# Optimization experiments

Hardware: AMD Instinct MI355X
Metric: run time of the kernel (lower is better)

The kernel has to match this reference:

```python
import jax, jax.numpy as jnp
import numpy as np

U, B, D = 1024, 8, 512
H, HD = 8, 64
CL, RC = 64, 4            # chunk length, right-context per chunk
C = U // CL               # 16 chunks
R, S, M = C * RC, C, C - 1
Q, KV = R + U + S, M + R + U
PE = 2 * U - 1
NEG_INF = -1e8


def _chunk_mask():
    # True = disallowed connection. Query rows = [right_context(R), utterance(U), summary(S)];
    # key cols = [memory(M), right_context(R), utterance(U)].
    mask = np.ones((Q, KV), dtype=bool)
    for c in range(C):
        cols = []
        cols += list(range(0, c))                                  # memory of preceding chunks
        cols += list(range(M + c * RC, M + (c + 1) * RC))          # own right context
        u0 = max(0, c - 1) * CL                                    # one left-context chunk
        cols += list(range(M + R + u0, M + R + (c + 1) * CL))      # utterance up to own chunk
        cols = np.array(cols)
        rows = np.concatenate([
            np.arange(c * RC, (c + 1) * RC),                       # right-context queries
            np.arange(R + c * CL, R + (c + 1) * CL),               # utterance queries
            np.array([R + U + c]),                                 # summary query
        ])
        mask[np.ix_(rows, cols)] = False
    return jnp.asarray(mask)


def _xavier(key, shape):
    fan_in, fan_out = shape[-1], shape[0]
    a = (6.0 / (fan_in + fan_out)) ** 0.5
    return jax.random.uniform(key, shape, jnp.float32, -a, a)


def setup_inputs() -> dict:
    key = jax.random.key(0)
    ks = jax.random.split(key, 16)
    return {
        "utterance": jax.random.normal(ks[0], (U, B, D), jnp.float32),
        "lengths": jax.random.randint(ks[1], (B,), U // 2, U + 1),
        "right_context": jax.random.normal(ks[2], (R, B, D), jnp.float32),
        "summary": jax.random.normal(ks[3], (S, B, D), jnp.float32),
        "memory": jax.random.normal(ks[4], (M, B, D), jnp.float32),
        "attention_mask": _chunk_mask(),
        "pos_emb": jax.random.normal(ks[5], (PE, D), jnp.float32),
        "W_kv": _xavier(ks[6], (2 * D, D)),
        "b_kv": jnp.zeros((2 * D,), jnp.float32),
        "W_q": _xavier(ks[7], (D, D)),
        "b_q": jnp.zeros((D,), jnp.float32),
        "W_out": _xavier(ks[8], (D, D)),
        "b_out": jnp.zeros((D,), jnp.float32),
        "W_pos": _xavier(ks[9], (D, D)),
        "pos_bias_u": _xavier(ks[10], (H, HD)),
        "pos_bias_v": _xavier(ks[11], (H, HD)),
    }


def reference(utterance, lengths, right_context, summary, memory, attention_mask,
              pos_emb, W_kv, b_kv, W_q, b_q, W_out, b_out, W_pos,
              pos_bias_u, pos_bias_v):
    u_len, b, d = utterance.shape
    r, m, s = right_context.shape[0], memory.shape[0], summary.shape[0]
    h = pos_bias_u.shape[0]
    hd = d // h
    scaling = hd ** -0.5

    query = jnp.concatenate([right_context, utterance, summary], 0) @ W_q.T + b_q   # (Q,B,D)
    kv = jnp.concatenate([memory, right_context, utterance], 0) @ W_kv.T + b_kv     # (KV,B,2D)
    key_t, val_t = kv[..., :d], kv[..., d:]
    q_len, kv_len = query.shape[0], key_t.shape[0]

    k = key_t.reshape(kv_len, b, h, hd).transpose(1, 2, 0, 3)   # (B,H,KV,hd)
    v = val_t.reshape(kv_len, b, h, hd).transpose(1, 2, 0, 3)   # (B,H,KV,hd)
    q = query.reshape(q_len, b, h, hd)                           # (Q,B,H,hd)

    qu = (q + pos_bias_u).transpose(1, 2, 0, 3)                  # (B,H,Q,hd)
    matrix_ac = jnp.einsum('bhqe,bhke->bhqk', qu, k)             # (B,H,Q,KV)

    qv = (q[r:r + u_len] + pos_bias_v).transpose(1, 2, 0, 3)     # (B,H,U,hd)
    pe_len = pos_emb.shape[0]
    pos = (pos_emb @ W_pos.T).reshape(pe_len, h, hd).transpose(1, 0, 2)  # (H,PE,hd)
    bd_u = jnp.einsum('bhue,hpe->bhup', qv, pos)                 # (B,H,U,PE)

    # rel_shift: out[u, j] = in[u, U-1-u+j]
    out_len = pe_len - (u_len - 1)
    idx = (u_len - 1) - jnp.arange(u_len)[:, None] + jnp.arange(out_len)[None, :]
    bd_u = jnp.take_along_axis(bd_u, idx[None, None], axis=-1)   # (B,H,U,out_len)

    matrix_bd = jnp.zeros_like(matrix_ac).at[:, :, r:r + u_len, m + r:].set(bd_u)
    w = (matrix_ac + matrix_bd) * scaling

    w = jnp.where(attention_mask[None, None], NEG_INF, w)
    pad = jnp.arange(kv_len)[None, :] >= (kv_len - u_len + lengths)[:, None]  # (B,KV)
    w = jnp.where(pad[:, None, None, :], NEG_INF, w)

    probs = jax.nn.softmax(w, axis=-1)
    attn = jnp.einsum('bhqk,bhke->bhqe', probs, v)               # (B,H,Q,hd)
    attn = attn.transpose(2, 0, 1, 3).reshape(q_len, b, d)       # (Q,B,D)

    out_ru = attn[:r + u_len] @ W_out.T + b_out                  # (R+U,B,D)
    out_mem = jnp.clip(attn[r + u_len:], -10.0, 10.0)            # (S,B,D); tanh_on_mem=False
    return out_ru, out_mem
```

## Files before the change

### kernel.cpp

```cpp
#include <hip/hip_runtime.h>
#include <hip/hip_bf16.h>

typedef __hip_bfloat16 bf16;
typedef __attribute__((ext_vector_type(8))) short short8v;
typedef __attribute__((ext_vector_type(4))) float float4v;

#define UU 1024
#define BB 8
#define DD 512
#define HH 8
#define HD 64
#define RR 64
#define SS 16
#define MM 15
#define QQ 1104
#define KVL 1103
#define PEL 2047
#define NU 1536
#define MU 8952

#define AS1 __attribute__((address_space(1)))
#define AS3 __attribute__((address_space(3)))

__device__ __forceinline__ float lo16(unsigned u) { return __uint_as_float(u << 16); }
__device__ __forceinline__ float hi16(unsigned u) { return __uint_as_float(u & 0xffff0000u); }
__device__ __forceinline__ unsigned pk2(float a, float b) {
  unsigned short x = __builtin_bit_cast(unsigned short, __float2bfloat16(a));
  unsigned short y = __builtin_bit_cast(unsigned short, __float2bfloat16(b));
  return (unsigned)x | ((unsigned)y << 16);
}

__device__ __forceinline__ void nt_st_bf16(bf16* p, float v) {
  bf16 t = __float2bfloat16(v);
  __builtin_nontemporal_store(__builtin_bit_cast(short, t), (short*)p);
}
__device__ __forceinline__ void nt_st_f32(float* p, float v) {
  __builtin_nontemporal_store(v, p);
}

struct PackDesc {
  const void* src[16];
  unsigned int srcoff[16];
  unsigned int dstoff[16];
  unsigned int cum[17];
};

__global__ __launch_bounds__(256) void pack_all(PackDesc d, bf16* base,
                                                const void* __restrict__ probe,
                                                int* __restrict__ flagout,
                                                int nchunks) {
  __shared__ int wsum[4];
  const unsigned short* p = (const unsigned short*)probe;
  int big = 0;
  for (int i = threadIdx.x; i < 4096; i += 256)
    big += (((p[i] >> 7) & 0xFF) >= 137) ? 1 : 0;
  #pragma unroll
  for (int off = 32; off; off >>= 1) big += __shfl_down(big, off);
  if ((threadIdx.x & 63) == 0) wsum[threadIdx.x >> 6] = big;
  __syncthreads();
  const int flag = (wsum[0] + wsum[1] + wsum[2] + wsum[3] < 16) ? 1 : 0;
  if (threadIdx.x == 0 && blockIdx.x == 0) *flagout = flag;

  int g = blockIdx.x * 256 + threadIdx.x;
  if (g >= nchunks) return;
  int s = 0;
  #pragma unroll
  for (int i = 1; i < 17; ++i) s += (g >= d.cum[i]) ? 1 : 0;
  unsigned local = (g - d.cum[s]) * 8u;
  bf16* dst = base + d.dstoff[s] + local;
  if (flag) {
    const uint4 v = *(const uint4*)((const bf16*)d.src[s] + d.srcoff[s] + local);
    *(uint4*)dst = v;
  } else {
    const float* fp = (const float*)d.src[s] + d.srcoff[s] + local;
    uint4 o;
    o.x = pk2(fp[0], fp[1]);
    o.y = pk2(fp[2], fp[3]);
    o.z = pk2(fp[4], fp[5]);
    o.w = pk2(fp[6], fp[7]);
    *(uint4*)dst = o;
  }
}

struct GemmP {
  const bf16* X; const bf16* W; const bf16* bias; void* out;
  int M, N, K; const int* outf;
};

__global__ __launch_bounds__(256, 3) void gemm_dual(GemmP g0, GemmP g1, int ysplit) {
  __shared__ bf16 As[64 * 128];
  __shared__ bf16 Bs[128 * 128];
  GemmP g; int bm, bn;
  if ((int)blockIdx.y < ysplit) {
    g = g0;
    int bi = (int)blockIdx.y * (int)gridDim.x + (int)blockIdx.x;
    int nbn = g0.N >> 7;
    int j = bi >> 3;
    int bmi = (bi & 7) + (j / nbn) * 8;
    int bni = j % nbn;
    if (bmi >= ((g0.M + 63) >> 6)) return;
    bm = bmi * 64; bn = bni * 128;
  } else {
    g = g1;
    int nt = g1.N >> 7;
    int bi = ((int)blockIdx.y - ysplit) * gridDim.x + blockIdx.x;
    if (bi >= ((g1.M + 63) >> 6) * nt) return;
    bm = (bi / nt) * 64; bn = (bi % nt) * 128;
  }
  const int tid = threadIdx.x;
  const int lane = tid & 63, wv = tid >> 6;
  const int wr = wv >> 1, wc = wv & 1;
  const int l4 = lane >> 4;
  const int lb = lane & 15;
  const int quad = lane >> 4, l15 = lane & 15;

  float4v acc[2][4] = {};

  for (int kb = 0; kb < g.K; kb += 128) {
    #pragma unroll
    for (int i = 0; i < 4; ++i) {
      int r = wv * 16 + i * 4 + l4;
      int gm = bm + r; if (gm > g.M - 1) gm = g.M - 1;
      const bf16* src = g.X + (size_t)gm * g.K + kb + ((lb ^ (r & 15)) * 8);
      __builtin_amdgcn_global_load_lds((const AS1 void*)src,
                                       (AS3 void*)&As[(wv * 16 + i * 4) * 128], 16, 0, 0);
    }
    #pragma unroll
    for (int i = 0; i < 8; ++i) {
      int r = wv * 32 + i * 4 + l4;
      int gn = bn + r; if (gn > g.N - 1) gn = g.N - 1;
      const bf16* src = g.W + (size_t)gn * g.K + kb + ((lb ^ (r & 15)) * 8);
      __builtin_amdgcn_global_load_lds((const AS1 void*)src,
                                       (AS3 void*)&Bs[(wv * 32 + i * 4) * 128], 16, 0, 0);
    }
    __syncthreads();
    #pragma unroll
    for (int ki = 0; ki < 4; ++ki) {
      const int slot = ((ki * 4 + quad) ^ l15) * 8;
      short8v a[2], bq[4];
      #pragma unroll
      for (int t = 0; t < 2; ++t)
        a[t] = *(const short8v*)&As[(wr * 32 + t * 16 + l15) * 128 + slot];
      #pragma unroll
      for (int t = 0; t < 4; ++t)
        bq[t] = *(const short8v*)&Bs[(wc * 64 + t * 16 + l15) * 128 + slot];
      #pragma unroll
      for (int mt = 0; mt < 2; ++mt)
        #pragma unroll
        for (int nt = 0; nt < 4; ++nt)
          acc[mt][nt] = __builtin_amdgcn_mfma_f32_16x16x32_bf16(
              a[mt], bq[nt], acc[mt][nt], 0, 0, 0);
    }
    __syncthreads();
  }

  const bool as_bf16 = (g.outf == nullptr) ? true : (*g.outf != 0);
  #pragma unroll
  for (int mt = 0; mt < 2; ++mt) {
    #pragma unroll
    for (int r = 0; r < 4; ++r) {
      int gm = bm + wr * 32 + mt * 16 + quad * 4 + r;
      if (gm >= g.M) continue;
      #pragma unroll
      for (int nt = 0; nt < 4; ++nt) {
        int gn = bn + wc * 64 + nt * 16 + l15;
        float v = acc[mt][nt][r];
        if (g.bias) v += __bfloat162float(g.bias[gn]);
        size_t o = (size_t)gm * g.N + gn;
        if (as_bf16) nt_st_bf16((bf16*)g.out + o, v);
        else         nt_st_f32((float*)g.out + o, v);
      }
    }
  }
}

__global__ __launch_bounds__(512, 2) void gemm8(
    const bf16* __restrict__ XUp, const bf16* __restrict__ Wcatp,
    const bf16* __restrict__ bcatp, bf16* __restrict__ qkvp,
    const bf16* __restrict__ posecp, const bf16* __restrict__ Wpospp,
    bf16* __restrict__ posp) {
  __shared__ bf16 smem[65536];
  const int tid = threadIdx.x;
  const int lane = tid & 63, wv = tid >> 6;
  const int wr = wv >> 2, wc = wv & 3;
  const int quad = lane >> 4, l15 = lane & 15;

  const bf16 *gX, *gW, *gB; bf16* gO; int gM, gN, bm, bn;
  const int bid = (int)blockIdx.x;
  if (bid < 210) {
    int xcd = bid & 7, j = bid >> 3;
    int wg = (xcd < 2 ? xcd * 27 : 54 + (xcd - 2) * 26) + j;
    bm = (wg / 6) * 256; bn = (wg % 6) * 256;
    gX = XUp; gW = Wcatp; gB = bcatp; gO = qkvp; gM = MU; gN = NU;
  } else {
    gX = posecp; gW = Wpospp; gB = nullptr; gO = posp; gM = 191; gN = 512;
    bm = 0; bn = (bid - 210) * 256;
  }

  bf16* A0 = smem;
  bf16* B0 = smem + 32768;

  auto stage = [&](const bf16* src, int rbase, int Mlim, bf16* dst, int kb) {
    #pragma unroll
    for (int j = 0; j < 2; ++j) {
      int rl = j * 128 + wv * 16 + (lane >> 2);
      int gr = rbase + rl; if (gr > Mlim - 1) gr = Mlim - 1;
      int kc = ((lane & 3) ^ ((rl >> 1) & 3)) * 8;
      const bf16* s = src + (size_t)gr * 512 + kb + kc;
      __builtin_amdgcn_global_load_lds((const AS1 void*)s,
                                       (AS3 void*)(dst + (j * 128 + wv * 16) * 32), 16, 0, 0);
    }
  };

  float4v acc[8][4] = {};
  const int pos8 = (quad ^ ((l15 >> 1) & 3)) * 8;

  stage(gX, bm, gM, A0, 0);          stage(gW, bn, gN, B0, 0);
  stage(gX, bm, gM, A0 + 8192, 32);  stage(gW, bn, gN, B0 + 8192, 32);
  stage(gX, bm, gM, A0 + 16384, 64); stage(gW, bn, gN, B0 + 16384, 64);
  asm volatile("s_waitcnt vmcnt(8)" ::: "memory");
  asm volatile("s_barrier" ::: "memory");

  #pragma unroll
  for (int s = 0; s < 16; ++s) {
    if (s + 3 < 16) {
      stage(gX, bm, gM, A0 + ((s + 3) & 3) * 8192, (s + 3) * 32);
      stage(gW, bn, gN, B0 + ((s + 3) & 3) * 8192, (s + 3) * 32);
    }
    const bf16* As = A0 + (s & 3) * 8192;
    const bf16* Bs = B0 + (s & 3) * 8192;
    short8v al[8], bl[4];
    #pragma unroll
    for (int i = 0; i < 8; ++i)
      al[i] = *(const short8v*)&As[(wr * 128 + i * 16 + l15) * 32 + pos8];
    #pragma unroll
    for (int j = 0; j < 4; ++j)
      bl[j] = *(const short8v*)&Bs[(wc * 64 + j * 16 + l15) * 32 + pos8];
    asm volatile("s_barrier" ::: "memory");
    __builtin_amdgcn_s_setprio(1);
    #pragma unroll
    for (int i = 0; i < 8; ++i)
      #pragma unroll
      for (int j = 0; j < 4; ++j)
        acc[i][j] = __builtin_amdgcn_mfma_f32_16x16x32_bf16(al[i], bl[j], acc[i][j], 0, 0, 0);
    __builtin_amdgcn_s_setprio(0);
    if (s <= 12)      asm volatile("s_waitcnt vmcnt(8)" ::: "memory");
    else if (s == 13) asm volatile("s_waitcnt vmcnt(4)" ::: "memory");
    else if (s == 14) asm volatile("s_waitcnt vmcnt(0)" ::: "memory");
    if (s < 15)       asm volatile("s_barrier" ::: "memory");
  }

  #pragma unroll
  for (int mf = 0; mf < 8; ++mf) {
    #pragma unroll
    for (int r = 0; r < 4; ++r) {
      int gm = bm + wr * 128 + mf * 16 + quad * 4 + r;
      if (gm >= gM) continue;
      #pragma unroll
      for (int nf = 0; nf < 4; ++nf) {
        int gn = bn + wc * 64 + nf * 16 + l15;
        float v = acc[mf][nf][r];
        if (gB) v += __bfloat162float(gB[gn]);
        gO[(size_t)gm * gN + gn] = __float2bfloat16(v);
      }
    }
  }
}

__device__ __forceinline__ int gcol(int row, int c, int u0, int ncols) {
  if (row < c) return row;
  if (row < c + 4) return 15 + 4 * c + (row - c);
  if (row < ncols) return 79 + u0 + (row - c - 4);
  return 0;
}

__global__ __launch_bounds__(256, 2) void attn_chunk(
    const bf16* __restrict__ qkv, const bf16* __restrict__ pos,
    const bf16* __restrict__ pbu, const bf16* __restrict__ pbv,
    const int* __restrict__ lengths, bf16* __restrict__ attn,
    const int* __restrict__ flag, void* __restrict__ dout) {
  __shared__ char lds[65536];
  bf16* Vs   = (bf16*)(lds);
  bf16* Aqu  = (bf16*)(lds + 19456);
  bf16* Kt   = (bf16*)(lds + 29696);
  bf16* Aqv  = (bf16*)(lds + 32768);
  bf16* Psl  = (bf16*)(lds + 40960);
  bf16* Eb   = (bf16*)(lds + 49152);
  bf16* Pp   = (bf16*)(lds + 19456);
  float* wred  = (float*)(lds + 46336);
  float* rstat = (float*)(lds + 47616);

  const int idx = blockIdx.x;
  const int h = idx & 7, b = (idx >> 3) & 7, c = idx >> 6;
  const int u0 = c ? (c - 1) * 64 : 0;
  const int nut = c ? 128 : 64;
  const int ncols = c + 4 + nut;
  const int q0 = c ? 63 : 127;
  const int tid = threadIdx.x, lane = tid & 63, wv = tid >> 6;
  const int quad = lane >> 4, l15 = lane & 15, key = l15 & 7;
  const int lenlim = lengths[b] - u0;
  const bool obf = (*flag != 0);

  {
    int lr = lane >> 3;
    int sbr = (lane & 7) ^ lr;
    for (int i = wv; i < 19; i += 4) {
      int row = i * 8 + lr;
      int g = gcol(row, c, u0, ncols);
      int sbv = (lane & 7) ^ (i & 7);
      const bf16* src = qkv + ((size_t)(g * 8 + b)) * NU + 1024 + h * 64 + sbv * 8;
      __builtin_amdgcn_global_load_lds((const AS1 void*)src, (AS3 void*)(Vs + i * 512), 16, 0, 0);
    }
    for (int i = wv; i < 24; i += 4) {
      int p = i * 8 + lr;
      const bf16* src = pos + (size_t)p * 512 + h * 64 + sbr * 8;
      __builtin_amdgcn_global_load_lds((const AS1 void*)src, (AS3 void*)(Psl + i * 512), 16, 0, 0);
    }
  }
  for (int id = tid; id < 1152; id += 256) {
    bool isv = id >= 640;
    int lid = isv ? id - 640 : id;
    int m = lid >> 3, ec = lid & 7;
    int qrow;
    if (isv) qrow = 64 + 64 * c + m;
    else qrow = (m < 64) ? (64 + 64 * c + m)
              : (m < 68) ? (4 * c + (m - 64))
              : (m == 68) ? (1088 + c) : 0;
    const uint4 qa = *(const uint4*)(qkv + ((size_t)((qrow + 15) * 8 + b)) * NU + h * 64 + ec * 8);
    const uint4 ba = *(const uint4*)((isv ? pbv : pbu) + h * 64 + ec * 8);
    uint4 o;
    o.x = pk2(lo16(qa.x) + lo16(ba.x), hi16(qa.x) + hi16(ba.x));
    o.y = pk2(lo16(qa.y) + lo16(ba.y), hi16(qa.y) + hi16(ba.y));
    o.z = pk2(lo16(qa.z) + lo16(ba.z), hi16(qa.z) + hi16(ba.z));
    o.w = pk2(lo16(qa.w) + lo16(ba.w), hi16(qa.w) + hi16(ba.w));
    *(uint4*)((isv ? Aqv : Aqu) + m * 64 + (ec ^ (m & 7)) * 8) = o;
  }
  __syncthreads();

  float4v eacc[4][3];
  #pragma unroll
  for (int mt = 0; mt < 4; ++mt)
    #pragma unroll
    for (int i = 0; i < 3; ++i) eacc[mt][i] = (float4v){0.f, 0.f, 0.f, 0.f};
  {
    short8v av[4][2];
    #pragma unroll
    for (int mt = 0; mt < 4; ++mt)
      #pragma unroll
      for (int ks = 0; ks < 2; ++ks)
        av[mt][ks] = *(const short8v*)&Aqv[(mt * 16 + l15) * 64 + ((ks * 4 + quad) ^ key) * 8];
    #pragma unroll
    for (int nti = 0; nti < 3; ++nti) {
      int nt = wv + nti * 4;
      short8v b0 = *(const short8v*)&Psl[(nt * 16 + l15) * 64 + (quad ^ key) * 8];
      short8v b1 = *(const short8v*)&Psl[(nt * 16 + l15) * 64 + ((4 + quad) ^ key) * 8];
      #pragma unroll
      for (int mt = 0; mt < 4; ++mt) {
        eacc[mt][nti] = __builtin_amdgcn_mfma_f32_16x16x32_bf16(av[mt][0], b0, eacc[mt][nti], 0, 0, 0);
        eacc[mt][nti] = __builtin_amdgcn_mfma_f32_16x16x32_bf16(av[mt][1], b1, eacc[mt][nti], 0, 0, 0);
      }
    }
  }
  __syncthreads();

  {
    int lr = lane >> 3, sbr = (lane & 7) ^ lr;
    for (int i = wv; i < 19; i += 4) {
      int row = i * 8 + lr;
      int g = gcol(row, c, u0, ncols);
      const bf16* src = qkv + ((size_t)(g * 8 + b)) * NU + 512 + h * 64 + sbr * 8;
      __builtin_amdgcn_global_load_lds((const AS1 void*)src, (AS3 void*)(Kt + i * 512), 16, 0, 0);
    }
  }
  #pragma unroll
  for (int nti = 0; nti < 3; ++nti) {
    int p = (wv + nti * 4) * 16 + l15;
    #pragma unroll
    for (int mt = 0; mt < 4; ++mt)
      #pragma unroll
      for (int r = 0; r < 4; ++r) {
        int m = mt * 16 + quad * 4 + r;
        int jl = p - q0 + m;
        if (jl >= 0 && jl < nut)
          Eb[m * 128 + (jl ^ (((m >> 2) & 7) << 4))] = __float2bfloat16(eacc[mt][nti][r]);
      }
  }
  __syncthreads();

  const int nnt = (wv < 2) ? 3 : 2;
  float4v sacc[5][3];
  #pragma unroll
  for (int mt = 0; mt < 5; ++mt)
    #pragma unroll
    for (int i = 0; i < 3; ++i) sacc[mt][i] = (float4v){0.f, 0.f, 0.f, 0.f};
  {
    short8v au[5][2];
    #pragma unroll
    for (int mt = 0; mt < 5; ++mt)
      #pragma unroll
      for (int ks = 0; ks < 2; ++ks)
        au[mt][ks] = *(const short8v*)&Aqu[(mt * 16 + l15) * 64 + ((ks * 4 + quad) ^ key) * 8];
    #pragma unroll
    for (int nti = 0; nti < 3; ++nti) {
      if (nti < nnt) {
        int nt = wv + nti * 4;
        short8v b0 = *(const short8v*)&Kt[(nt * 16 + l15) * 64 + (quad ^ key) * 8];
        short8v b1 = *(const short8v*)&Kt[(nt * 16 + l15) * 64 + ((4 + quad) ^ key) * 8];
        #pragma unroll
        for (int mt = 0; mt < 5; ++mt) {
          sacc[mt][nti] = __builtin_amdgcn_mfma_f32_16x16x32_bf16(au[mt][0], b0, sacc[mt][nti], 0, 0, 0);
          sacc[mt][nti] = __builtin_amdgcn_mfma_f32_16x16x32_bf16(au[mt][1], b1, sacc[mt][nti], 0, 0, 0);
        }
      }
    }
  }
  __syncthreads();

  #pragma unroll
  for (int nti = 0; nti < 3; ++nti) {
    if (nti < nnt) {
      int colv = (wv + nti * 4) * 16 + l15;
      int jl = colv - (c + 4);
      bool cvalid = (colv < ncols) && !(jl >= 0 && jl >= lenlim);
      #pragma unroll
      for (int mt = 0; mt < 5; ++mt)
        #pragma unroll
        for (int r = 0; r < 4; ++r) {
          float s = sacc[mt][nti][r];
          if (cvalid) {
            if (mt < 4 && jl >= 0) {
              int m = mt * 16 + quad * 4 + r;
              s += __bfloat162float(Eb[m * 128 + (jl ^ (((m >> 2) & 7) << 4))]);
            }
            s *= 0.125f;
          } else s = -1e30f;
          sacc[mt][nti][r] = s;
        }
    }
  }

  {
    #pragma unroll
    for (int mt = 0; mt < 5; ++mt)
      #pragma unroll
      for (int r = 0; r < 4; ++r) {
        float v = -3e38f;
        #pragma unroll
        for (int nti = 0; nti < 3; ++nti)
          if (nti < nnt) v = fmaxf(v, sacc[mt][nti][r]);
        v = fmaxf(v, __shfl_xor(v, 1));
        v = fmaxf(v, __shfl_xor(v, 2));
        v = fmaxf(v, __shfl_xor(v, 4));
        v = fmaxf(v, __shfl_xor(v, 8));
        if (l15 == 0) wred[(mt * 16 + quad * 4 + r) * 4 + wv] = v;
      }
  }
  __syncthreads();
  if (tid < 80)
    rstat[tid] = fmaxf(fmaxf(wred[tid * 4], wred[tid * 4 + 1]),
                       fmaxf(wred[tid * 4 + 2], wred[tid * 4 + 3]));
  __syncthreads();

  {
    float rmx[5][4], rsum[5][4];
    #pragma unroll
    for (int mt = 0; mt < 5; ++mt)
      #pragma unroll
      for (int r = 0; r < 4; ++r) {
        rmx[mt][r] = rstat[mt * 16 + quad * 4 + r];
        rsum[mt][r] = 0.f;
      }
    #pragma unroll
    for (int nti = 0; nti < 3; ++nti) {
      if (nti < nnt) {
        int colv = (wv + nti * 4) * 16 + l15;
        #pragma unroll
        for (int mt = 0; mt < 5; ++mt)
          #pragma unroll
          for (int r = 0; r < 4; ++r) {
            float p = __expf(sacc[mt][nti][r] - rmx[mt][r]);
            Pp[(mt * 16 + quad * 4 + r) * 168 + colv] = __float2bfloat16(p);
            rsum[mt][r] += p;
          }
      }
    }
    #pragma unroll
    for (int mt = 0; mt < 5; ++mt)
      #pragma unroll
      for (int r = 0; r < 4; ++r) {
        float v = rsum[mt][r];
        v += __shfl_xor(v, 1);
        v += __shfl_xor(v, 2);
        v += __shfl_xor(v, 4);
        v += __shfl_xor(v, 8);
        if (l15 == 0) wred[(mt * 16 + quad * 4 + r) * 4 + wv] = v;
      }
  }
  __syncthreads();
  if (tid < 80)
    rstat[tid] = 1.f / (wred[tid * 4] + wred[tid * 4 + 1] + wred[tid * 4 + 2] + wred[tid * 4 + 3]);
  __syncthreads();

  const int kmax = (ncols + 31) >> 5;
  float4v oacc[5];
  #pragma unroll
  for (int mt = 0; mt < 5; ++mt) oacc[mt] = (float4v){0.f, 0.f, 0.f, 0.f};
  const int ehi = (wv * 16 + l15) >> 3, elo = l15 & 7;
  for (int ks = 0; ks < kmax; ++ks) {
    short8v bq;
    const int blk = ehi ^ ((ks * 4 + quad) & 7);
    #pragma unroll
    for (int j = 0; j < 8; ++j)
      bq[j] = ((const short*)Vs)[(ks * 32 + quad * 8 + j) * 64 + blk * 8 + elo];
    #pragma unroll
    for (int mt = 0; mt < 5; ++mt) {
      short8v af = *(const short8v*)&Pp[(mt * 16 + l15) * 168 + ks * 32 + quad * 8];
      oacc[mt] = __builtin_amdgcn_mfma_f32_16x16x32_bf16(af, bq, oacc[mt], 0, 0, 0);
    }
  }

  #pragma unroll
  for (int mt = 0; mt < 5; ++mt) {
    #pragma unroll
    for (int r = 0; r < 4; ++r) {
      int m = mt * 16 + quad * 4 + r;
      if (m >= 69) continue;
      float o = oacc[mt][r] * rstat[m];
      if (m < 68) {
        int qrow = (m < 64) ? (64 + 64 * c + m) : (4 * c + (m - 64));
        attn[((size_t)(qrow * 8 + b)) * 512 + h * 64 + wv * 16 + l15] = __float2bfloat16(o);
      } else {
        float v = fminf(fmaxf(o, -10.f), 10.f);
        size_t oi = (size_t)1088 * 8 * 512 + ((size_t)(c * 8 + b)) * 512 + h * 64 + wv * 16 + l15;
        if (obf) nt_st_bf16((bf16*)dout + oi, v);
        else     nt_st_f32((float*)dout + oi, v);
      }
    }
  }
}

static inline int cdiv(int a, int b) { return (a + b - 1) / b; }

extern "C" void kernel_launch(void* const* d_in, const int* in_sizes, int n_in,
                              void* d_out, int out_size, void* d_ws, size_t ws_size,
                              hipStream_t stream) {
  const void* utter = d_in[0];
  const int*  lens  = (const int*)d_in[1];
  const void* rctx  = d_in[2];
  const void* summ  = d_in[3];
  const void* memry = d_in[4];
  const void* pose  = d_in[6];
  const void* W_kv  = d_in[7];
  const void* b_kv  = d_in[8];
  const void* W_q   = d_in[9];
  const void* b_q   = d_in[10];
  const void* W_out = d_in[11];
  const void* b_out = d_in[12];
  const void* W_pos = d_in[13];
  const void* pbu   = d_in[14];
  const void* pbv   = d_in[15];

  const unsigned SZ_MM = MM * BB * DD;
  const unsigned SZ_RC = RR * BB * DD;
  const unsigned SZ_UT = UU * BB * DD;
  const unsigned SZ_SM = SS * BB * DD;
  const unsigned N_XU  = SZ_MM + SZ_RC + SZ_UT + SZ_SM;
  const unsigned SZ_PS = 191 * DD;

  int*  flag = (int*)d_ws;
  bf16* base = (bf16*)((char*)d_ws + 64);
  unsigned off = 0;
  bf16* XU    = base + off; unsigned o_XU    = off; off += N_XU;
  bf16* posec = base + off; unsigned o_posec = off; off += 192 * DD;
  bf16* Wcat  = base + off; unsigned o_Wcat  = off; off += (unsigned)NU * DD;
  bf16* bcat  = base + off; unsigned o_bcat  = off; off += NU;
  bf16* Woutp = base + off; unsigned o_Wout  = off; off += DD * DD;
  bf16* boutp = base + off; unsigned o_bout  = off; off += DD;
  bf16* Wposp = base + off; unsigned o_Wpos  = off; off += DD * DD;
  bf16* pbuc  = base + off; unsigned o_pbu   = off; off += DD;
  bf16* pbvc  = base + off; unsigned o_pbv   = off; off += DD;
  bf16* qkv   = base + off; off += (unsigned)(MU + 8) * NU;
  bf16* pos   = base + off; off += 192 * DD;
  bf16* attn  = base + off; off += QQ * BB * DD;

  PackDesc pd;
  const void* srcs[14]  = {memry, rctx, utter, summ, pose,
                           W_q, W_kv, b_q, b_kv, W_out, b_out, W_pos, pbu, pbv};
  unsigned    soffs[14] = {0, 0, 0, 0, 896u * DD, 0, 0, 0, 0, 0, 0, 0, 0, 0};
  unsigned    doffs[14] = {o_XU, o_XU + SZ_MM, o_XU + SZ_MM + SZ_RC,
                           o_XU + SZ_MM + SZ_RC + SZ_UT, o_posec,
                           o_Wcat, o_Wcat + DD * DD, o_bcat, o_bcat + DD,
                           o_Wout, o_bout, o_Wpos, o_pbu, o_pbv};
  unsigned    ns[14]    = {SZ_MM, SZ_RC, SZ_UT, SZ_SM, SZ_PS,
                           DD * DD, 2 * DD * DD, DD, 2 * DD,
                           DD * DD, DD, DD * DD, DD, DD};
  unsigned cum = 0;
  for (int i = 0; i < 14; ++i) {
    pd.src[i] = srcs[i]; pd.srcoff[i] = soffs[i]; pd.dstoff[i] = doffs[i];
    pd.cum[i] = cum; cum += ns[i] / 8;
  }
  pd.src[14] = pbv; pd.srcoff[14] = 0; pd.dstoff[14] = o_pbv;
  pd.src[15] = pbv; pd.srcoff[15] = 0; pd.dstoff[15] = o_pbv;
  pd.cum[14] = cum; pd.cum[15] = cum; pd.cum[16] = cum;
  int nchunks = (int)cum;
  pack_all<<<dim3(cdiv(nchunks, 256)), dim3(256), 0, stream>>>(pd, base, utter, flag, nchunks);

  gemm8<<<dim3(212), dim3(512), 0, stream>>>(XU, Wcat, bcat, qkv, posec, Wposp, pos);

  attn_chunk<<<dim3(1024), dim3(256), 0, stream>>>(qkv, pos, pbuc, pbvc, lens, attn,
                                                   flag, d_out);

  GemmP go{attn, Woutp, boutp, d_out, (RR + UU) * BB, DD, DD, flag};
  gemm_dual<<<dim3(4, 136), dim3(256), 0, stream>>>(go, go, 136);
}
```

Baseline: 196.7 us.

## Partition attention score tiles by query rows per wave to avoid cross-wave softmax reductions

Work in the chunk attention kernel is now split across waves by query-row tile instead of key-column tile. Each wave computes a full row of scores, with the key-column loop bounded by the actual column count, so softmax max and sum reductions stay within the wave. This removes the LDS scratch round-trip and several __syncthreads barriers. The cost is load imbalance: with five row tiles over four waves, wave 0 does two tiles while the others do one, and it raises per-wave accumulator register use.

```diff
diff --git a/kernel.cpp b/kernel.cpp
--- a/kernel.cpp
+++ b/kernel.cpp
@@ -287,7 +287,6 @@
   bf16* Psl  = (bf16*)(lds + 40960);
   bf16* Eb   = (bf16*)(lds + 49152);
   bf16* Pp   = (bf16*)(lds + 19456);
-  float* wred  = (float*)(lds + 46336);
   float* rstat = (float*)(lds + 47616);
 
   const int idx = blockIdx.x;
@@ -300,6 +299,7 @@
   const int quad = lane >> 4, l15 = lane & 15, key = l15 & 7;
   const int lenlim = lengths[b] - u0;
   const bool obf = (*flag != 0);
+  const int ktp = ((ncols + 31) >> 5) * 2;
 
   {
     int lr = lane >> 3;
@@ -337,28 +337,20 @@
   }
   __syncthreads();
 
-  float4v eacc[4][3];
-  #pragma unroll
-  for (int mt = 0; mt < 4; ++mt)
-    #pragma unroll
-    for (int i = 0; i < 3; ++i) eacc[mt][i] = (float4v){0.f, 0.f, 0.f, 0.f};
+  float4v eacc[12];
+  #pragma unroll
+  for (int i = 0; i < 12; ++i) eacc[i] = (float4v){0.f, 0.f, 0.f, 0.f};
   {
-    short8v av[4][2];
-    #pragma unroll
-    for (int mt = 0; mt < 4; ++mt)
-      #pragma unroll
-      for (int ks = 0; ks < 2; ++ks)
-        av[mt][ks] = *(const short8v*)&Aqv[(mt * 16 + l15) * 64 + ((ks * 4 + quad) ^ key) * 8];
-    #pragma unroll
-    for (int nti = 0; nti < 3; ++nti) {
-      int nt = wv + nti * 4;
-      short8v b0 = *(const short8v*)&Psl[(nt * 16 + l15) * 64 + (quad ^ key) * 8];
-      short8v b1 = *(const short8v*)&Psl[(nt * 16 + l15) * 64 + ((4 + quad) ^ key) * 8];
-      #pragma unroll
-      for (int mt = 0; mt < 4; ++mt) {
-        eacc[mt][nti] = __builtin_amdgcn_mfma_f32_16x16x32_bf16(av[mt][0], b0, eacc[mt][nti], 0, 0, 0);
-        eacc[mt][nti] = __builtin_amdgcn_mfma_f32_16x16x32_bf16(av[mt][1], b1, eacc[mt][nti], 0, 0, 0);
-      }
+    short8v av[2];
+    #pragma unroll
+    for (int ks = 0; ks < 2; ++ks)
+      av[ks] = *(const short8v*)&Aqv[(wv * 16 + l15) * 64 + ((ks * 4 + quad) ^ key) * 8];
+    #pragma unroll
+    for (int nti = 0; nti < 12; ++nti) {
+      short8v b0 = *(const short8v*)&Psl[(nti * 16 + l15) * 64 + (quad ^ key) * 8];
+      short8v b1 = *(const short8v*)&Psl[(nti * 16 + l15) * 64 + ((4 + quad) ^ key) * 8];
+      eacc[nti] = __builtin_amdgcn_mfma_f32_16x16x32_bf16(av[0], b0, eacc[nti], 0, 0, 0);
+      eacc[nti] = __builtin_amdgcn_mfma_f32_16x16x32_bf16(av[1], b1, eacc[nti], 0, 0, 0);
     }
   }
   __syncthreads();
@@ -373,132 +365,133 @@
     }
   }
   #pragma unroll
-  for (int nti = 0; nti < 3; ++nti) {
-    int p = (wv + nti * 4) * 16 + l15;
-    #pragma unroll
-    for (int mt = 0; mt < 4; ++mt)
-      #pragma unroll
-      for (int r = 0; r < 4; ++r) {
-        int m = mt * 16 + quad * 4 + r;
-        int jl = p - q0 + m;
-        if (jl >= 0 && jl < nut)
-          Eb[m * 128 + (jl ^ (((m >> 2) & 7) << 4))] = __float2bfloat16(eacc[mt][nti][r]);
-      }
+  for (int nti = 0; nti < 12; ++nti) {
+    int p = nti * 16 + l15;
+    #pragma unroll
+    for (int r = 0; r < 4; ++r) {
+      int m = wv * 16 + quad * 4 + r;
+      int jl = p - q0 + m;
+      if (jl >= 0 && jl < nut)
+        Eb[m * 128 + (jl ^ (((m >> 2) & 7) << 4))] = __float2bfloat16(eacc[nti][r]);
+    }
   }
   __syncthreads();
 
-  const int nnt = (wv < 2) ? 3 : 2;
-  float4v sacc[5][3];
-  #pragma unroll
-  for (int mt = 0; mt < 5; ++mt)
-    #pragma unroll
-    for (int i = 0; i < 3; ++i) sacc[mt][i] = (float4v){0.f, 0.f, 0.f, 0.f};
+  float4v sacc[2][10];
+  #pragma unroll
+  for (int ti = 0; ti < 2; ++ti)
+    #pragma unroll
+    for (int i = 0; i < 10; ++i) sacc[ti][i] = (float4v){0.f, 0.f, 0.f, 0.f};
   {
-    short8v au[5][2];
-    #pragma unroll
-    for (int mt = 0; mt < 5; ++mt)
-      #pragma unroll
-      for (int ks = 0; ks < 2; ++ks)
-        au[mt][ks] = *(const short8v*)&Aqu[(mt * 16 + l15) * 64 + ((ks * 4 + quad) ^ key) * 8];
-    #pragma unroll
-    for (int nti = 0; nti < 3; ++nti) {
-      if (nti < nnt) {
-        int nt = wv + nti * 4;
-        short8v b0 = *(const short8v*)&Kt[(nt * 16 + l15) * 64 + (quad ^ key) * 8];
-        short8v b1 = *(const short8v*)&Kt[(nt * 16 + l15) * 64 + ((4 + quad) ^ key) * 8];
+    short8v au[2][2];
+    #pragma unroll
+    for (int ti = 0; ti < 2; ++ti) {
+      int tt = wv + ti * 4;
+      if (tt < 5) {
         #pragma unroll
-        for (int mt = 0; mt < 5; ++mt) {
-          sacc[mt][nti] = __builtin_amdgcn_mfma_f32_16x16x32_bf16(au[mt][0], b0, sacc[mt][nti], 0, 0, 0);
-          sacc[mt][nti] = __builtin_amdgcn_mfma_f32_16x16x32_bf16(au[mt][1], b1, sacc[mt][nti], 0, 0, 0);
+        for (int ks = 0; ks < 2; ++ks)
+          au[ti][ks] = *(const short8v*)&Aqu[(tt * 16 + l15) * 64 + ((ks * 4 + quad) ^ key) * 8];
+      }
+    }
+    #pragma unroll
+    for (int nti = 0; nti < 10; ++nti) {
+      if (nti < ktp) {
+        short8v b0 = *(const short8v*)&Kt[(nti * 16 + l15) * 64 + (quad ^ key) * 8];
+        short8v b1 = *(const short8v*)&Kt[(nti * 16 + l15) * 64 + ((4 + quad) ^ key) * 8];
+        #pragma unroll
+        for (int ti = 0; ti < 2; ++ti) {
+          int tt = wv + ti * 4;
+          if (tt < 5) {
+            sacc[ti][nti] = __builtin_amdgcn_mfma_f32_16x16x32_bf16(au[ti][0], b0, sacc[ti][nti], 0, 0, 0);
+            sacc[ti][nti] = __builtin_amdgcn_mfma_f32_16x16x32_bf16(au[ti][1], b1, sacc[ti][nti], 0, 0, 0);
+          }
         }
       }
     }
   }
-  __syncthreads();
-
-  #pragma unroll
-  for (int nti = 0; nti < 3; ++nti) {
-    if (nti < nnt) {
-      int colv = (wv + nti * 4) * 16 + l15;
+
+  #pragma unroll
+  for (int nti = 0; nti < 10; ++nti) {
+    if (nti < ktp) {
+      int colv = nti * 16 + l15;
       int jl = colv - (c + 4);
       bool cvalid = (colv < ncols) && !(jl >= 0 && jl >= lenlim);
       #pragma unroll
-      for (int mt = 0; mt < 5; ++mt)
-        #pragma unroll
-        for (int r = 0; r < 4; ++r) {
-          float s = sacc[mt][nti][r];
-          if (cvalid) {
-            if (mt < 4 && jl >= 0) {
-              int m = mt * 16 + quad * 4 + r;
-              s += __bfloat162float(Eb[m * 128 + (jl ^ (((m >> 2) & 7) << 4))]);
-            }
-            s *= 0.125f;
-          } else s = -1e30f;
-          sacc[mt][nti][r] = s;
+      for (int ti = 0; ti < 2; ++ti) {
+        int tt = wv + ti * 4;
+        if (tt < 5) {
+          #pragma unroll
+          for (int r = 0; r < 4; ++r) {
+            float s = sacc[ti][nti][r];
+            if (cvalid) {
+              if (tt < 4 && jl >= 0) {
+                int m = tt * 16 + quad * 4 + r;
+                s += __bfloat162float(Eb[m * 128 + (jl ^ (((m >> 2) & 7) << 4))]);
+              }
+              s *= 0.125f;
+            } else s = -1e30f;
+            sacc[ti][nti][r] = s;
+          }
         }
-    }
-  }
-
-  {
-    #pragma unroll
-    for (int mt = 0; mt < 5; ++mt)
+      }
+    }
+  }
+
+  float rmx[2][4], rsum[2][4];
+  #pragma unroll
+  for (int ti = 0; ti < 2; ++ti) {
+    int tt = wv + ti * 4;
+    if (tt < 5) {
       #pragma unroll
       for (int r = 0; r < 4; ++r) {
         float v = -3e38f;
         #pragma unroll
-        for (int nti = 0; nti < 3; ++nti)
-          if (nti < nnt) v = fmaxf(v, sacc[mt][nti][r]);
+        for (int nti = 0; nti < 10; ++nti)
+          if (nti < ktp) v = fmaxf(v, sacc[ti][nti][r]);
         v = fmaxf(v, __shfl_xor(v, 1));
         v = fmaxf(v, __shfl_xor(v, 2));
         v = fmaxf(v, __shfl_xor(v, 4));
         v = fmaxf(v, __shfl_xor(v, 8));
-        if (l15 == 0) wred[(mt * 16 + quad * 4 + r) * 4 + wv] = v;
-      }
+        rmx[ti][r] = v;
+        rsum[ti][r] = 0.f;
+      }
+    }
   }
   __syncthreads();
-  if (tid < 80)
-    rstat[tid] = fmaxf(fmaxf(wred[tid * 4], wred[tid * 4 + 1]),
-                       fmaxf(wred[tid * 4 + 2], wred[tid * 4 + 3]));
-  __syncthreads();
-
-  {
-    float rmx[5][4], rsum[5][4];
-    #pragma unroll
-    for (int mt = 0; mt < 5; ++mt)
-      #pragma unroll
-      for (int r = 0; r < 4; ++r) {
-        rmx[mt][r] = rstat[mt * 16 + quad * 4 + r];
-        rsum[mt][r] = 0.f;
-      }
-    #pragma unroll
-    for (int nti = 0; nti < 3; ++nti) {
-      if (nti < nnt) {
-        int colv = (wv + nti * 4) * 16 + l15;
-        #pragma unroll
-        for (int mt = 0; mt < 5; ++mt)
+
+  #pragma unroll
+  for (int nti = 0; nti < 10; ++nti) {
+    if (nti < ktp) {
+      int colv = nti * 16 + l15;
+      #pragma unroll
+      for (int ti = 0; ti < 2; ++ti) {
+        int tt = wv + ti * 4;
+        if (tt < 5) {
           #pragma unroll
           for (int r = 0; r < 4; ++r) {
-            float p = __expf(sacc[mt][nti][r] - rmx[mt][r]);
-            Pp[(mt * 16 + quad * 4 + r) * 168 + colv] = __float2bfloat16(p);
-            rsum[mt][r] += p;
+            float p = __expf(sacc[ti][nti][r] - rmx[ti][r]);
+            Pp[(tt * 16 + quad * 4 + r) * 168 + colv] = __float2bfloat16(p);
+            rsum[ti][r] += p;
           }
-      }
-    }
-    #pragma unroll
-    for (int mt = 0; mt < 5; ++mt)
+        }
+      }
+    }
+  }
+  #pragma unroll
+  for (int ti = 0; ti < 2; ++ti) {
+    int tt = wv + ti * 4;
+    if (tt < 5) {
       #pragma unroll
       for (int r = 0; r < 4; ++r) {
-        float v = rsum[mt][r];
+        float v = rsum[ti][r];
         v += __shfl_xor(v, 1);
         v += __shfl_xor(v, 2);
         v += __shfl_xor(v, 4);
         v += __shfl_xor(v, 8);
-        if (l15 == 0) wred[(mt * 16 + quad * 4 + r) * 4 + wv] = v;
-      }
-  }
-  __syncthreads();
-  if (tid < 80)
-    rstat[tid] = 1.f / (wred[tid * 4] + wred[tid * 4 + 1] + wred[tid * 4 + 2] + wred[tid * 4 + 3]);
+        if (l15 == 0) rstat[tt * 16 + quad * 4 + r] = 1.f / v;
+      }
+    }
+  }
   __syncthreads();
 
   const int kmax = (ncols + 31) >> 5;
```

Measured after the change: 193.1 us. Within noise of the previous version (-1.8%).
